# Optimization experiments

Hardware: AMD Instinct MI355X
Metric: run time of the kernel (lower is better)

Reference implementation:

```python
import jax, jax.numpy as jnp
import numpy as np
from jax import lax

HEADS = 8
LN_EPS = 1e-5


def setup_inputs() -> dict:
    key = jax.random.key(0)
    k = jax.random.split(key, 8)
    B, C, H, W, r = 4, 64, 64, 64, 4
    T = H * W
    x = jax.random.normal(k[0], (B, C, H, W), dtype=jnp.float32)
    conv_w = jax.random.normal(k[1], (C, C, r, r), dtype=jnp.float32) * 0.02  # OIHW
    conv_b = jnp.zeros((C,), dtype=jnp.float32)
    ln_g = jnp.ones((C,), dtype=jnp.float32)
    ln_b = jnp.zeros((C,), dtype=jnp.float32)
    Wqkv = jax.random.normal(k[2], (C, 3 * C), dtype=jnp.float32) * 0.02  # to_qvk (no bias)
    W0 = jax.random.normal(k[3], (C, C), dtype=jnp.float32) * 0.02  # output proj (no bias)
    E = jax.random.normal(k[4], (T, T // 4), dtype=jnp.float32)  # Linformer proj (randn in torch fwd)
    return {"x": x, "conv_w": conv_w, "conv_b": conv_b, "ln_g": ln_g,
            "ln_b": ln_b, "Wqkv": Wqkv, "W0": W0, "E": E}


def _layernorm2d(y, g, b):
    # LayerNorm over channel dim of NCHW (torch: permute to NHWC, LN last dim)
    yt = y.transpose(0, 2, 3, 1)  # b h w c
    mu = yt.mean(-1, keepdims=True)
    var = ((yt - mu) ** 2).mean(-1, keepdims=True)
    yt = (yt - mu) * lax.rsqrt(var + LN_EPS) * g + b
    return yt.transpose(0, 3, 1, 2)


def reference(x, conv_w, conv_b, ln_g, ln_b, Wqkv, W0, E):
    B, C, H, W = x.shape
    T = H * W
    dh = C // HEADS
    r = conv_w.shape[-1]

    # reducer: conv(stride=r) + LayerNorm2d. NOTE: faithful to the torch module,
    # this result is computed but NEVER used by the output (dead code in source).
    red = lax.conv_general_dilated(x, conv_w, (r, r), 'VALID',
                                   dimension_numbers=('NCHW', 'OIHW', 'NCHW'))
    red = red + conv_b[None, :, None, None]
    _red = _layernorm2d(red, ln_g, ln_b)  # unused, matches source

    # tokens from full-resolution x: b c h w -> b (h w) c
    xf = x.reshape(B, C, T).transpose(0, 2, 1)  # [B,T,C]
    qkv = xf @ Wqkv  # [B,T,3C]
    # rearrange 'b t (d k h)' with k=3, h=HEADS -> composite order (d, k, h)
    qkv = qkv.reshape(B, T, dh, 3, HEADS)
    q = qkv[:, :, :, 0, :].transpose(0, 3, 1, 2)  # [B,h,T,d]
    kk = qkv[:, :, :, 1, :].transpose(0, 3, 1, 2)
    v = qkv[:, :, :, 2, :].transpose(0, 3, 1, 2)

    # Linformer low-rank projection of V and K: [B,h,T,d] x [T,k] -> [B,h,k,d]
    v = jnp.einsum('bhjd,jk->bhkd', v, E)
    kk = jnp.einsum('bhjd,jk->bhkd', kk, E)

    scale = dh ** -0.5
    scores = jnp.einsum('bhid,bhjd->bhij', q, kk) * scale  # [B,h,T,k]
    attn = jax.nn.softmax(scores, axis=-1)
    out = jnp.einsum('bhij,bhjd->bhid', attn, v)  # [B,h,T,d]

    out = out.transpose(0, 2, 1, 3).reshape(B, T, C)  # b h i d -> b i (h d)
    out = out @ W0  # [B,T,C]
    return out.transpose(0, 2, 1).reshape(B, C, H, W)
```

## Files before the change

### kernel.cpp

```cpp
#include <hip/hip_runtime.h>

#define T_DIM 4096
#define KD    1024
#define SCALE2 (0.35355339059327373f * 1.4426950408889634f)
#define VT_PITCH 1032

extern "C" __device__ float __ocml_native_exp2_f32(float);

typedef __attribute__((ext_vector_type(8))) short bf16x8;
typedef __attribute__((ext_vector_type(4))) float f32x4;
typedef __attribute__((ext_vector_type(16))) float f32x16;

__device__ inline unsigned short f2bf(float f) {
  unsigned u = __float_as_uint(f);
  unsigned r = u + 0x7fffu + ((u >> 16) & 1u);
  return (unsigned short)(r >> 16);
}

__device__ inline unsigned cvt_pk_bf16(float a, float b) {
  unsigned ua = __float_as_uint(a); ua += 0x7fffu + ((ua >> 16) & 1u);
  unsigned ub = __float_as_uint(b); ub += 0x7fffu + ((ub >> 16) & 1u);
  return (ua >> 16) | (ub & 0xffff0000u);
}

__device__ inline bf16x8 mk8(unsigned a, unsigned b, unsigned c, unsigned d) {
  union { unsigned u[4]; bf16x8 v; } x;
  x.u[0] = a; x.u[1] = b; x.u[2] = c; x.u[3] = d; return x.v;
}

__global__ __launch_bounds__(256) void k_front(const float* __restrict__ x,
                                               const float* __restrict__ E,
                                               const float* __restrict__ Wqkv,
                                               float* __restrict__ partial,
                                               float* __restrict__ Q,
                                               float* __restrict__ out) {
  const int bid = blockIdx.x;
  const int tid = threadIdx.x;

  ((float4*)out)[(size_t)bid * 256 + tid] = make_float4(0.f, 0.f, 0.f, 0.f);

  if (bid < 512) {
    const int kb = bid & 15;
    const int b  = (bid >> 4) & 3;
    const int s  = bid >> 6;
    const int lane = tid & 63;
    const int w = tid >> 6;
    const int li = lane & 15, lg = lane >> 4;
    const int kcol = kb * 64 + w * 16 + li;

    f32x4 acc[4] = {};
#pragma unroll 2
    for (int tb = 0; tb < 16; ++tb) {
      const int tbase = s * 512 + tb * 32 + lg * 8;
      float bv[8];
#pragma unroll
      for (int j = 0; j < 8; ++j)
        bv[j] = E[(size_t)(tbase + j) * KD + kcol];
      bf16x8 bq = mk8(cvt_pk_bf16(bv[0], bv[1]), cvt_pk_bf16(bv[2], bv[3]),
                      cvt_pk_bf16(bv[4], bv[5]), cvt_pk_bf16(bv[6], bv[7]));
#pragma unroll
      for (int mt = 0; mt < 4; ++mt) {
        const float* ap = x + ((size_t)b * 64 + mt * 16 + li) * T_DIM + tbase;
        float4 a0 = *(const float4*)(ap);
        float4 a1 = *(const float4*)(ap + 4);
        bf16x8 af8 = mk8(cvt_pk_bf16(a0.x, a0.y), cvt_pk_bf16(a0.z, a0.w),
                         cvt_pk_bf16(a1.x, a1.y), cvt_pk_bf16(a1.z, a1.w));
        acc[mt] = __builtin_amdgcn_mfma_f32_16x16x32_bf16(af8, bq, acc[mt], 0, 0, 0);
      }
    }
    float* pb = partial + ((size_t)s * 4 + b) * (64 * KD);
#pragma unroll
    for (int mt = 0; mt < 4; ++mt) {
      const int row = mt * 16 + lg * 4;
#pragma unroll
      for (int reg = 0; reg < 4; ++reg)
        pb[(size_t)(row + reg) * KD + kcol] = acc[mt][reg];
    }
  } else {
    const int idx = bid - 512;
    const int g  = idx & 7;
    const int tt = (idx >> 3) & 15;
    const int b  = idx >> 7;
    const int t  = tt * 256 + tid;
    const int col0 = g * 24;

    float acc[8];
#pragma unroll
    for (int j = 0; j < 8; ++j) acc[j] = 0.f;
    const float* xb = x + (size_t)b * 64 * T_DIM + t;
#pragma unroll 4
    for (int c = 0; c < 64; ++c) {
      float xv = xb[(size_t)c * T_DIM];
      const float* wr = Wqkv + c * 192 + col0;
#pragma unroll
      for (int h = 0; h < 8; ++h) acc[h] += xv * wr[h];
    }
#pragma unroll
    for (int h = 0; h < 8; ++h)
      Q[(((size_t)(b * 8 + h)) * 8 + g) * T_DIM + t] = acc[h];
  }
}

__global__ __launch_bounds__(256) void k_xkv(const float* __restrict__ partial,
                                             const float* __restrict__ Wqkv,
                                             uint2* __restrict__ Kg,
                                             unsigned short* __restrict__ Vg) {
  __shared__ float XPs[64 * 64];
  const int kb = blockIdx.x;
  const int h  = blockIdx.y;
  const int b  = blockIdx.z;
  const int tid = threadIdx.x;

  {
    const int kk = tid & 63;
    const int cg = tid >> 6;
#pragma unroll 4
    for (int u = 0; u < 16; ++u) {
      const int c = cg * 16 + u;
      const size_t src = (size_t)c * KD + kb * 64 + kk;
      float a = 0.f;
#pragma unroll
      for (int s = 0; s < 8; ++s)
        a += partial[((size_t)s * 4 + b) * (64 * KD) + src];
      XPs[c * 64 + kk] = a;
    }
  }
  __syncthreads();

  const int klocal = tid & 63;
  const int sel    = (tid >> 6) & 1;
  const int dg     = tid >> 7;
  const int k      = kb * 64 + klocal;

  float acc[4];
#pragma unroll
  for (int d = 0; d < 4; ++d) acc[d] = 0.f;
#pragma unroll 8
  for (int c = 0; c < 64; ++c) {
    float xv = XPs[c * 64 + klocal];
    const float* wr = Wqkv + c * 192 + (sel + 1) * 8 + h;
#pragma unroll
    for (int d = 0; d < 4; ++d) acc[d] += xv * wr[(dg * 4 + d) * 24];
  }

  const int bh = b * 8 + h;
  if (sel == 0) {
    uint2* kg = Kg + (size_t)bh * 2048;
    kg[k * 2 + dg] = make_uint2(cvt_pk_bf16(acc[0] * SCALE2, acc[1] * SCALE2),
                                cvt_pk_bf16(acc[2] * SCALE2, acc[3] * SCALE2));
  } else {
#pragma unroll
    for (int d = 0; d < 4; ++d)
      Vg[(size_t)(bh * 8 + dg * 4 + d) * KD + k] = f2bf(acc[d]);
  }
}

__global__ __launch_bounds__(256, 4) void k_attn(const float* __restrict__ Q,
                                              const uint2* __restrict__ Kg,
                                              const unsigned short* __restrict__ Vg,
                                              const float* __restrict__ W0,
                                              float* __restrict__ out) {
  __shared__ __attribute__((aligned(16))) unsigned short Kt[1024 * 8];
  __shared__ unsigned short Vt[9 * VT_PITCH];
  __shared__ float W0s[512];
  const int bh = blockIdx.x;
  const int tid = threadIdx.x;
  const int b = bh >> 3, h = bh & 7;

  const uint4* kg4 = (const uint4*)(Kg + (size_t)bh * 2048);
  uint4* kt4 = (uint4*)Kt;
#pragma unroll
  for (int it = 0; it < 4; ++it)
    kt4[it * 256 + tid] = kg4[it * 256 + tid];
  const unsigned* vg = (const unsigned*)(Vg + (size_t)bh * 8192);
#pragma unroll
  for (int dd = 0; dd < 8; ++dd) {
#pragma unroll
    for (int it = 0; it < 2; ++it) {
      const int j2 = it * 256 + tid;
      *(unsigned*)(Vt + dd * VT_PITCH + j2 * 2) = vg[dd * 512 + j2];
    }
  }
#pragma unroll
  for (int it = 0; it < 2; ++it)
    *(unsigned*)(Vt + 8 * VT_PITCH + (it * 256 + tid) * 2) = 0x3F803F80u;
  W0s[tid]       = W0[h * 512 + tid];
  W0s[tid + 256] = W0[h * 512 + tid + 256];
  __syncthreads();

  const int lane = tid & 63, w = tid >> 6;
  const int icol = lane & 31, half = lane >> 5;
  const int i0w = blockIdx.y * 128 + w * 32;

  bf16x8 qf8 = {};
  if (lane < 32) {
    const float* qp = Q + (size_t)bh * 8 * T_DIM + i0w + icol;
    float q0 = qp[0],          q1 = qp[T_DIM],     q2 = qp[2 * T_DIM];
    float q3 = qp[3 * T_DIM],  q4 = qp[4 * T_DIM], q5 = qp[5 * T_DIM];
    float q6 = qp[6 * T_DIM],  q7 = qp[7 * T_DIM];
    qf8 = mk8(cvt_pk_bf16(q0, q1), cvt_pk_bf16(q2, q3),
              cvt_pk_bf16(q4, q5), cvt_pk_bf16(q6, q7));
  }

  f32x16 accO = {};
  for (int jt = 0; jt < 1024; jt += 32) {
    bf16x8 kf8 = {};
    if (lane < 32) kf8 = *(const bf16x8*)(&Kt[(jt + lane) * 8]);
    f32x16 z = {};
    f32x16 st = __builtin_amdgcn_mfma_f32_32x32x16_bf16(kf8, qf8, z, 0, 0, 0);

    unsigned e0, e1, e2, e3, e4, e5, e6, e7;
    {
      float p0  = __ocml_native_exp2_f32(st[0]),  p1  = __ocml_native_exp2_f32(st[1]);
      float p2  = __ocml_native_exp2_f32(st[2]),  p3  = __ocml_native_exp2_f32(st[3]);
      float p4  = __ocml_native_exp2_f32(st[4]),  p5  = __ocml_native_exp2_f32(st[5]);
      float p6  = __ocml_native_exp2_f32(st[6]),  p7  = __ocml_native_exp2_f32(st[7]);
      float p8  = __ocml_native_exp2_f32(st[8]),  p9  = __ocml_native_exp2_f32(st[9]);
      float p10 = __ocml_native_exp2_f32(st[10]), p11 = __ocml_native_exp2_f32(st[11]);
      float p12 = __ocml_native_exp2_f32(st[12]), p13 = __ocml_native_exp2_f32(st[13]);
      float p14 = __ocml_native_exp2_f32(st[14]), p15 = __ocml_native_exp2_f32(st[15]);
      asm("v_cvt_pk_bf16_f32 %0, %1, %2" : "=v"(e0) : "v"(p0),  "v"(p1));
      asm("v_cvt_pk_bf16_f32 %0, %1, %2" : "=v"(e1) : "v"(p2),  "v"(p3));
      asm("v_cvt_pk_bf16_f32 %0, %1, %2" : "=v"(e2) : "v"(p4),  "v"(p5));
      asm("v_cvt_pk_bf16_f32 %0, %1, %2" : "=v"(e3) : "v"(p6),  "v"(p7));
      asm("v_cvt_pk_bf16_f32 %0, %1, %2" : "=v"(e4) : "v"(p8),  "v"(p9));
      asm("v_cvt_pk_bf16_f32 %0, %1, %2" : "=v"(e5) : "v"(p10), "v"(p11));
      asm("v_cvt_pk_bf16_f32 %0, %1, %2" : "=v"(e6) : "v"(p12), "v"(p13));
      asm("v_cvt_pk_bf16_f32 %0, %1, %2" : "=v"(e7) : "v"(p14), "v"(p15));
    }
    asm("v_permlane32_swap_b32 %0, %1" : "+v"(e0), "+v"(e2));
    asm("v_permlane32_swap_b32 %0, %1" : "+v"(e1), "+v"(e3));
    asm("v_permlane32_swap_b32 %0, %1" : "+v"(e4), "+v"(e6));
    asm("v_permlane32_swap_b32 %0, %1" : "+v"(e5), "+v"(e7));

    bf16x8 va0 = {}, va1 = {};
    if (icol < 9) {
      const unsigned short* vp = Vt + icol * VT_PITCH + jt + half * 8;
      va0 = *(const bf16x8*)(vp);
      va1 = *(const bf16x8*)(vp + 16);
    }
    accO = __builtin_amdgcn_mfma_f32_32x32x16_bf16(va0, mk8(e0, e1, e2, e3), accO, 0, 0, 0);
    accO = __builtin_amdgcn_mfma_f32_32x32x16_bf16(va1, mk8(e4, e5, e6, e7), accO, 0, 0, 0);
  }

  __syncthreads();
  float* OwW = (float*)Kt + w * 256;

  {
    float inv = 1.0f / __shfl(accO[4], icol);
    float4 o = make_float4(accO[0] * inv, accO[1] * inv,
                           accO[2] * inv, accO[3] * inv);
    *(float4*)(OwW + icol * 8 + half * 4) = o;
  }

  const int tok = icol, ch = half;
  float ov[8];
#pragma unroll
  for (int d = 0; d < 8; ++d) ov[d] = OwW[tok * 8 + d];
#pragma unroll 4
  for (int j = 0; j < 32; ++j) {
    const int c = ch * 32 + j;
    float a = 0.f;
#pragma unroll
    for (int d = 0; d < 8; ++d) a += ov[d] * W0s[d * 64 + c];
    atomicAdd(out + ((size_t)b * 64 + c) * T_DIM + i0w + tok, a);
  }
}

extern "C" void kernel_launch(void* const* d_in, const int* in_sizes, int n_in,
                              void* d_out, int out_size, void* d_ws, size_t ws_size,
                              hipStream_t stream) {
  const float* x    = (const float*)d_in[0];
  const float* Wqkv = (const float*)d_in[5];
  const float* W0   = (const float*)d_in[6];
  const float* E    = (const float*)d_in[7];
  float* out = (float*)d_out;

  float* Q           = (float*)d_ws;
  float* partial     = Q + 1048576;
  uint2* Kg          = (uint2*)(partial + 2097152);
  unsigned short* Vg = (unsigned short*)(Kg + 65536);

  k_front <<<dim3(1024),     256, 0, stream>>>(x, E, Wqkv, partial, Q, out);
  k_xkv   <<<dim3(16, 8, 4), 256, 0, stream>>>(partial, Wqkv, Kg, Vg);
  k_attn  <<<dim3(32, 32),   256, 0, stream>>>(Q, Kg, Vg, W0, out);
}
```

Before: 157.7 us.

## Stage x tile in LDS as bf16 and widen E-projection tiles per block

The x·E projection blocks now split T into 16 slices of 256 instead of 8 of 512, and each block covers 128 K columns instead of 64. The block's x slice is converted to bf16 once and staged in shared memory, then reused across two MFMA N-tiles per wave. This cuts the redundant global loads and conversions of x. In exchange, the split-K partial buffer doubles, so the reduce kernel sums 16 partials instead of 8 and the workspace offsets shift.

```diff
diff --git a/kernel.cpp b/kernel.cpp
--- a/kernel.cpp
+++ b/kernel.cpp
@@ -4,6 +4,7 @@
 #define KD    1024
 #define SCALE2 (0.35355339059327373f * 1.4426950408889634f)
 #define VT_PITCH 1032
+#define XS_PITCH 264
 
 extern "C" __device__ float __ocml_native_exp2_f32(float);
 
@@ -34,48 +35,68 @@
                                                float* __restrict__ partial,
                                                float* __restrict__ Q,
                                                float* __restrict__ out) {
+  __shared__ unsigned short xs[64 * XS_PITCH];
   const int bid = blockIdx.x;
   const int tid = threadIdx.x;
 
   ((float4*)out)[(size_t)bid * 256 + tid] = make_float4(0.f, 0.f, 0.f, 0.f);
 
   if (bid < 512) {
-    const int kb = bid & 15;
-    const int b  = (bid >> 4) & 3;
-    const int s  = bid >> 6;
+    const int kb = bid & 7;
+    const int b  = (bid >> 3) & 3;
+    const int s  = bid >> 5;
+    const int k0 = kb * 128;
     const int lane = tid & 63;
     const int w = tid >> 6;
     const int li = lane & 15, lg = lane >> 4;
-    const int kcol = kb * 64 + w * 16 + li;
-
-    f32x4 acc[4] = {};
+
+    {
+      const int tl = (tid & 127) * 2;
+      const int ch = tid >> 7;
+      const float* xb = x + ((size_t)b * 64 + ch) * T_DIM + s * 256 + tl;
+#pragma unroll 8
+      for (int it = 0; it < 32; ++it) {
+        const int c = it * 2 + ch;
+        float2 v = *(const float2*)(xb + (size_t)(it * 2) * T_DIM);
+        *(unsigned*)(&xs[c * XS_PITCH + tl]) = cvt_pk_bf16(v.x, v.y);
+      }
+    }
+    __syncthreads();
+
+    f32x4 acc[4][2] = {};
 #pragma unroll 2
-    for (int tb = 0; tb < 16; ++tb) {
-      const int tbase = s * 512 + tb * 32 + lg * 8;
-      float bv[8];
-#pragma unroll
-      for (int j = 0; j < 8; ++j)
-        bv[j] = E[(size_t)(tbase + j) * KD + kcol];
-      bf16x8 bq = mk8(cvt_pk_bf16(bv[0], bv[1]), cvt_pk_bf16(bv[2], bv[3]),
-                      cvt_pk_bf16(bv[4], bv[5]), cvt_pk_bf16(bv[6], bv[7]));
+    for (int tb = 0; tb < 8; ++tb) {
+      const int tbase = s * 256 + tb * 32 + lg * 8;
+      const int tloc  = tb * 32 + lg * 8;
+      bf16x8 bq[2];
+#pragma unroll
+      for (int nt = 0; nt < 2; ++nt) {
+        const int kcol = k0 + w * 32 + nt * 16 + li;
+        float bv[8];
+#pragma unroll
+        for (int j = 0; j < 8; ++j)
+          bv[j] = E[(size_t)(tbase + j) * KD + kcol];
+        bq[nt] = mk8(cvt_pk_bf16(bv[0], bv[1]), cvt_pk_bf16(bv[2], bv[3]),
+                     cvt_pk_bf16(bv[4], bv[5]), cvt_pk_bf16(bv[6], bv[7]));
+      }
 #pragma unroll
       for (int mt = 0; mt < 4; ++mt) {
-        const float* ap = x + ((size_t)b * 64 + mt * 16 + li) * T_DIM + tbase;
-        float4 a0 = *(const float4*)(ap);
-        float4 a1 = *(const float4*)(ap + 4);
-        bf16x8 af8 = mk8(cvt_pk_bf16(a0.x, a0.y), cvt_pk_bf16(a0.z, a0.w),
-                         cvt_pk_bf16(a1.x, a1.y), cvt_pk_bf16(a1.z, a1.w));
-        acc[mt] = __builtin_amdgcn_mfma_f32_16x16x32_bf16(af8, bq, acc[mt], 0, 0, 0);
+        bf16x8 af8 = *(const bf16x8*)(&xs[(mt * 16 + li) * XS_PITCH + tloc]);
+        acc[mt][0] = __builtin_amdgcn_mfma_f32_16x16x32_bf16(af8, bq[0], acc[mt][0], 0, 0, 0);
+        acc[mt][1] = __builtin_amdgcn_mfma_f32_16x16x32_bf16(af8, bq[1], acc[mt][1], 0, 0, 0);
       }
     }
     float* pb = partial + ((size_t)s * 4 + b) * (64 * KD);
 #pragma unroll
-    for (int mt = 0; mt < 4; ++mt) {
-      const int row = mt * 16 + lg * 4;
-#pragma unroll
-      for (int reg = 0; reg < 4; ++reg)
-        pb[(size_t)(row + reg) * KD + kcol] = acc[mt][reg];
-    }
+    for (int mt = 0; mt < 4; ++mt)
+#pragma unroll
+      for (int nt = 0; nt < 2; ++nt) {
+        const int row = mt * 16 + lg * 4;
+        const int col = k0 + w * 32 + nt * 16 + li;
+#pragma unroll
+        for (int reg = 0; reg < 4; ++reg)
+          pb[(size_t)(row + reg) * KD + col] = acc[mt][nt][reg];
+      }
   } else {
     const int idx = bid - 512;
     const int g  = idx & 7;
@@ -120,7 +141,7 @@
       const size_t src = (size_t)c * KD + kb * 64 + kk;
       float a = 0.f;
 #pragma unroll
-      for (int s = 0; s < 8; ++s)
+      for (int s = 0; s < 16; ++s)
         a += partial[((size_t)s * 4 + b) * (64 * KD) + src];
       XPs[c * 64 + kk] = a;
     }
@@ -278,7 +299,7 @@
 
   float* Q           = (float*)d_ws;
   float* partial     = Q + 1048576;
-  uint2* Kg          = (uint2*)(partial + 2097152);
+  uint2* Kg          = (uint2*)(partial + 4194304);
   unsigned short* Vg = (unsigned short*)(Kg + 65536);
 
   k_front <<<dim3(1024),     256, 0, stream>>>(x, E, Wqkv, partial, Q, out);
```

Result: slower. 161.2 us (+2.2%).

## Fuse K/V projection into front kernel, drop split-T partial sums

Applied to the files above, without the earlier changes.

The x·E reduction is now done over the full T dimension in each block: x tiles are staged in shared memory as bf16, partial results are reduced across waves in LDS, and the Wkv projection is applied in the same kernel. This removes the partial-sum buffer in global memory and the separate k_xkv launch. Each block now loops serially over all of T, which gives only 256 reduction blocks and a longer critical path. s_setprio is also raised around the MFMAs in the attention loop.

```diff
diff --git a/kernel.cpp b/kernel.cpp
--- a/kernel.cpp
+++ b/kernel.cpp
@@ -4,6 +4,9 @@
 #define KD    1024
 #define SCALE2 (0.35355339059327373f * 1.4426950408889634f)
 #define VT_PITCH 1032
+#define XS_PITCH 264
+#define XP_PITCH 17
+#define WK_PITCH 136
 
 extern "C" __device__ float __ocml_native_exp2_f32(float);
 
@@ -28,61 +31,121 @@
   x.u[0] = a; x.u[1] = b; x.u[2] = c; x.u[3] = d; return x.v;
 }
 
-__global__ __launch_bounds__(256) void k_front(const float* __restrict__ x,
+__global__ __launch_bounds__(512) void k_front(const float* __restrict__ x,
                                                const float* __restrict__ E,
                                                const float* __restrict__ Wqkv,
-                                               float* __restrict__ partial,
+                                               uint2* __restrict__ Kg,
+                                               unsigned short* __restrict__ Vg,
                                                float* __restrict__ Q,
                                                float* __restrict__ out) {
+  __shared__ __attribute__((aligned(16))) float SMEM[8 * 64 * XP_PITCH];
+  __shared__ __attribute__((aligned(16))) float Wkvs[64 * WK_PITCH];
+  unsigned short* xs = (unsigned short*)SMEM;
+  float* XPs = SMEM;
+
   const int bid = blockIdx.x;
   const int tid = threadIdx.x;
 
-  ((float4*)out)[(size_t)bid * 256 + tid] = make_float4(0.f, 0.f, 0.f, 0.f);
-
-  if (bid < 512) {
-    const int kb = bid & 15;
-    const int b  = (bid >> 4) & 3;
-    const int s  = bid >> 6;
-    const int lane = tid & 63;
-    const int w = tid >> 6;
+  if (bid < 256) {
+    const int kb = bid >> 2;
+    const int b  = bid & 3;
+    const int k0 = kb * 16;
+    const int lane = tid & 63, w = tid >> 6;
     const int li = lane & 15, lg = lane >> 4;
-    const int kcol = kb * 64 + w * 16 + li;
+
+#pragma unroll
+    for (int i = 0; i < 16; ++i) {
+      const int idx = tid + i * 512;
+      const int c = idx >> 7, j = idx & 127;
+      const int cg = j >> 3, d = j & 7;
+      const int sel = (cg < 8) ? 1 : 2, h = cg & 7;
+      Wkvs[c * WK_PITCH + j] = Wqkv[c * 192 + sel * 8 + h + d * 24];
+    }
 
     f32x4 acc[4] = {};
-#pragma unroll 2
-    for (int tb = 0; tb < 16; ++tb) {
-      const int tbase = s * 512 + tb * 32 + lg * 8;
+    const int tl  = (tid & 127) * 2;
+    const int chp = tid >> 7;
+    const int tloc = w * 32 + lg * 8;
+
+    for (int ct = 0; ct < 16; ++ct) {
+      const float* xb = x + ((size_t)b * 64 + chp) * T_DIM + ct * 256 + tl;
+#pragma unroll 4
+      for (int it = 0; it < 16; ++it) {
+        const int c = it * 4 + chp;
+        float2 v = *(const float2*)(xb + (size_t)(it * 4) * T_DIM);
+        *(unsigned*)(&xs[c * XS_PITCH + tl]) = cvt_pk_bf16(v.x, v.y);
+      }
+      __syncthreads();
+
+      const int tb = ct * 256 + tloc;
       float bv[8];
 #pragma unroll
       for (int j = 0; j < 8; ++j)
-        bv[j] = E[(size_t)(tbase + j) * KD + kcol];
+        bv[j] = E[(size_t)(tb + j) * KD + k0 + li];
       bf16x8 bq = mk8(cvt_pk_bf16(bv[0], bv[1]), cvt_pk_bf16(bv[2], bv[3]),
                       cvt_pk_bf16(bv[4], bv[5]), cvt_pk_bf16(bv[6], bv[7]));
 #pragma unroll
       for (int mt = 0; mt < 4; ++mt) {
-        const float* ap = x + ((size_t)b * 64 + mt * 16 + li) * T_DIM + tbase;
-        float4 a0 = *(const float4*)(ap);
-        float4 a1 = *(const float4*)(ap + 4);
-        bf16x8 af8 = mk8(cvt_pk_bf16(a0.x, a0.y), cvt_pk_bf16(a0.z, a0.w),
-                         cvt_pk_bf16(a1.x, a1.y), cvt_pk_bf16(a1.z, a1.w));
+        bf16x8 af8 = *(const bf16x8*)(&xs[(mt * 16 + li) * XS_PITCH + tloc]);
         acc[mt] = __builtin_amdgcn_mfma_f32_16x16x32_bf16(af8, bq, acc[mt], 0, 0, 0);
       }
-    }
-    float* pb = partial + ((size_t)s * 4 + b) * (64 * KD);
-#pragma unroll
-    for (int mt = 0; mt < 4; ++mt) {
-      const int row = mt * 16 + lg * 4;
-#pragma unroll
-      for (int reg = 0; reg < 4; ++reg)
-        pb[(size_t)(row + reg) * KD + kcol] = acc[mt][reg];
+      __syncthreads();
+    }
+
+#pragma unroll
+    for (int mt = 0; mt < 4; ++mt)
+#pragma unroll
+      for (int r = 0; r < 4; ++r)
+        XPs[(w * 64 + mt * 16 + lg * 4 + r) * XP_PITCH + li] = acc[mt][r];
+    __syncthreads();
+
+#pragma unroll
+    for (int i = 0; i < 2; ++i) {
+      const int idx = tid + i * 512;
+      const int c = idx >> 4, k = idx & 15;
+      float s = 0.f;
+#pragma unroll
+      for (int wp = 0; wp < 8; ++wp) s += XPs[(wp * 64 + c) * XP_PITCH + k];
+      XPs[c * XP_PITCH + k] = s;
+    }
+    __syncthreads();
+
+    {
+      const int k  = tid & 15;
+      const int cg = (tid >> 4) & 15;
+      const int dh = tid >> 8;
+      float a4[4] = {0.f, 0.f, 0.f, 0.f};
+#pragma unroll 8
+      for (int c = 0; c < 64; ++c) {
+        const float xv = XPs[c * XP_PITCH + k];
+        const float4 wv = *(const float4*)(&Wkvs[c * WK_PITCH + cg * 8 + dh * 4]);
+        a4[0] += xv * wv.x; a4[1] += xv * wv.y;
+        a4[2] += xv * wv.z; a4[3] += xv * wv.w;
+      }
+      const int h = cg & 7, bh = b * 8 + h, kk2 = k0 + k;
+      if (cg < 8) {
+        Kg[(size_t)bh * 2048 + kk2 * 2 + dh] =
+            make_uint2(cvt_pk_bf16(a4[0] * SCALE2, a4[1] * SCALE2),
+                       cvt_pk_bf16(a4[2] * SCALE2, a4[3] * SCALE2));
+      } else {
+#pragma unroll
+        for (int d = 0; d < 4; ++d)
+          Vg[(size_t)(bh * 8 + dh * 4 + d) * KD + kk2] = f2bf(a4[d]);
+      }
     }
   } else {
-    const int idx = bid - 512;
+    const int idx = bid - 256;
     const int g  = idx & 7;
-    const int tt = (idx >> 3) & 15;
-    const int b  = idx >> 7;
-    const int t  = tt * 256 + tid;
+    const int tt = (idx >> 3) & 7;
+    const int b  = idx >> 6;
+    const int t  = tt * 512 + tid;
     const int col0 = g * 24;
+
+    {
+      float4* o4 = (float4*)out;
+      o4[(size_t)idx * 1024 + tid]       = make_float4(0.f, 0.f, 0.f, 0.f);
+      o4[(size_t)idx * 1024 + tid + 512] = make_float4(0.f, 0.f, 0.f, 0.f);
+    }
 
     float acc[8];
 #pragma unroll
@@ -98,60 +161,6 @@
 #pragma unroll
     for (int h = 0; h < 8; ++h)
       Q[(((size_t)(b * 8 + h)) * 8 + g) * T_DIM + t] = acc[h];
-  }
-}
-
-__global__ __launch_bounds__(256) void k_xkv(const float* __restrict__ partial,
-                                             const float* __restrict__ Wqkv,
-                                             uint2* __restrict__ Kg,
-                                             unsigned short* __restrict__ Vg) {
-  __shared__ float XPs[64 * 64];
-  const int kb = blockIdx.x;
-  const int h  = blockIdx.y;
-  const int b  = blockIdx.z;
-  const int tid = threadIdx.x;
-
-  {
-    const int kk = tid & 63;
-    const int cg = tid >> 6;
-#pragma unroll 4
-    for (int u = 0; u < 16; ++u) {
-      const int c = cg * 16 + u;
-      const size_t src = (size_t)c * KD + kb * 64 + kk;
-      float a = 0.f;
-#pragma unroll
-      for (int s = 0; s < 8; ++s)
-        a += partial[((size_t)s * 4 + b) * (64 * KD) + src];
-      XPs[c * 64 + kk] = a;
-    }
-  }
-  __syncthreads();
-
-  const int klocal = tid & 63;
-  const int sel    = (tid >> 6) & 1;
-  const int dg     = tid >> 7;
-  const int k      = kb * 64 + klocal;
-
-  float acc[4];
-#pragma unroll
-  for (int d = 0; d < 4; ++d) acc[d] = 0.f;
-#pragma unroll 8
-  for (int c = 0; c < 64; ++c) {
-    float xv = XPs[c * 64 + klocal];
-    const float* wr = Wqkv + c * 192 + (sel + 1) * 8 + h;
-#pragma unroll
-    for (int d = 0; d < 4; ++d) acc[d] += xv * wr[(dg * 4 + d) * 24];
-  }
-
-  const int bh = b * 8 + h;
-  if (sel == 0) {
-    uint2* kg = Kg + (size_t)bh * 2048;
-    kg[k * 2 + dg] = make_uint2(cvt_pk_bf16(acc[0] * SCALE2, acc[1] * SCALE2),
-                                cvt_pk_bf16(acc[2] * SCALE2, acc[3] * SCALE2));
-  } else {
-#pragma unroll
-    for (int d = 0; d < 4; ++d)
-      Vg[(size_t)(bh * 8 + dg * 4 + d) * KD + k] = f2bf(acc[d]);
   }
 }
 
@@ -207,7 +216,9 @@
     bf16x8 kf8 = {};
     if (lane < 32) kf8 = *(const bf16x8*)(&Kt[(jt + lane) * 8]);
     f32x16 z = {};
+    __builtin_amdgcn_s_setprio(1);
     f32x16 st = __builtin_amdgcn_mfma_f32_32x32x16_bf16(kf8, qf8, z, 0, 0, 0);
+    __builtin_amdgcn_s_setprio(0);
 
     unsigned e0, e1, e2, e3, e4, e5, e6, e7;
     {
@@ -239,8 +250,10 @@
       va0 = *(const bf16x8*)(vp);
       va1 = *(const bf16x8*)(vp + 16);
     }
+    __builtin_amdgcn_s_setprio(1);
     accO = __builtin_amdgcn_mfma_f32_32x32x16_bf16(va0, mk8(e0, e1, e2, e3), accO, 0, 0, 0);
     accO = __builtin_amdgcn_mfma_f32_32x32x16_bf16(va1, mk8(e4, e5, e6, e7), accO, 0, 0, 0);
+    __builtin_amdgcn_s_setprio(0);
   }
 
   __syncthreads();
@@ -277,11 +290,9 @@
   float* out = (float*)d_out;
 
   float* Q           = (float*)d_ws;
-  float* partial     = Q + 1048576;
-  uint2* Kg          = (uint2*)(partial + 2097152);
+  uint2* Kg          = (uint2*)(Q + 1048576);
   unsigned short* Vg = (unsigned short*)(Kg + 65536);
 
-  k_front <<<dim3(1024),     256, 0, stream>>>(x, E, Wqkv, partial, Q, out);
-  k_xkv   <<<dim3(16, 8, 4), 256, 0, stream>>>(partial, Wqkv, Kg, Vg);
-  k_attn  <<<dim3(32, 32),   256, 0, stream>>>(Q, Kg, Vg, W0, out);
-}
+  k_front <<<dim3(512),    512, 0, stream>>>(x, E, Wqkv, Kg, Vg, Q, out);
+  k_attn  <<<dim3(32, 32), 256, 0, stream>>>(Q, Kg, Vg, W0, out);
+}
```

Measured after the change: 156.6 us. About the same (-0.7%).
